# Optimization experiments

Measured on AMD Instinct MI355X. Metric: run time of the kernel, lower is better.

Reference implementation:

```python
import jax, jax.numpy as jnp
import numpy as np

N_NODES = 100_000
N_EDGES = 1_600_000
IN_CH = 128
HIDDEN = 48
OUT_CH = 16
NEG_SLOPE = 0.2  # PyG GATConv default LeakyReLU slope


def setup_inputs() -> dict:
    key = jax.random.key(0)
    ks = jax.random.split(key, 8)
    x = jax.random.normal(ks[0], (N_NODES, IN_CH), dtype=jnp.float32)
    edge_index = jax.random.randint(ks[1], (2, N_EDGES), 0, N_NODES, dtype=jnp.int64)
    W = jax.random.normal(ks[2], (IN_CH, HIDDEN), dtype=jnp.float32) / np.sqrt(IN_CH)
    att_src = jax.random.normal(ks[3], (HIDDEN,), dtype=jnp.float32) / np.sqrt(HIDDEN)
    att_dst = jax.random.normal(ks[4], (HIDDEN,), dtype=jnp.float32) / np.sqrt(HIDDEN)
    gat_bias = jax.random.normal(ks[5], (HIDDEN,), dtype=jnp.float32) * 0.01
    lin_W = jax.random.normal(ks[6], (HIDDEN, OUT_CH), dtype=jnp.float32) / np.sqrt(HIDDEN)
    lin_b = jax.random.normal(ks[7], (OUT_CH,), dtype=jnp.float32) * 0.01
    return {"x": x, "edge_index": edge_index, "W": W, "att_src": att_src,
            "att_dst": att_dst, "gat_bias": gat_bias, "lin_W": lin_W, "lin_b": lin_b}


def reference(x, edge_index, W, att_src, att_dst, gat_bias, lin_W, lin_b):
    n = x.shape[0]
    # PyG GATConv adds self loops by default
    loops = jnp.arange(n, dtype=edge_index.dtype)
    src = jnp.concatenate([edge_index[0], loops])  # [E+N] message sources j
    dst = jnp.concatenate([edge_index[1], loops])  # [E+N] message targets i

    h = x @ W                      # [N, H] transformed node features
    a_src = h @ att_src            # [N] per-node source attention term
    a_dst = h @ att_dst            # [N] per-node destination attention term

    logits = jax.nn.leaky_relu(a_src[src] + a_dst[dst], NEG_SLOPE)  # [E+N]
    # segment softmax over incoming edges of each destination node
    m = jax.ops.segment_max(logits, dst, num_segments=n)            # [N]
    e = jnp.exp(logits - m[dst])
    denom = jax.ops.segment_sum(e, dst, num_segments=n)             # [N] (>0: self loop)
    alpha = e / denom[dst]                                          # [E+N]

    agg = jax.ops.segment_sum(h[src] * alpha[:, None], dst, num_segments=n)
    out = jax.nn.elu(agg + gat_bias)          # [N, H]
    # dropout is identity in eval mode
    z = out @ lin_W + lin_b                   # [N, OUT]
    return jax.nn.log_softmax(z, axis=-1)
```

## Files before the change

### kernel.cpp

```cpp
#include <hip/hip_runtime.h>
#include <hip/hip_fp16.h>

#define IN_CH 128
#define HID 48
#define OUT_CH 16
#define NEG_SLOPE 0.2f
#define SCAN_ELEMS 2048
#define ROWB 128

__device__ __forceinline__ float leaky(float x) { return x >= 0.f ? x : NEG_SLOPE * x; }
__device__ __forceinline__ float elu(float x) { return x > 0.f ? x : __expf(x) - 1.f; }

__device__ __forceinline__ void load_edge(const void* ei, int E, int is64, int e,
                                          int& s, int& d) {
    if (is64) {
        const long long* p = (const long long*)ei;
        s = (int)p[e];
        d = (int)p[(size_t)E + e];
    } else {
        const int* p = (const int*)ei;
        s = p[e];
        d = p[(size_t)E + e];
    }
}

#define BLK_NODES 256
__global__ __launch_bounds__(256, 2) void k_xw(const float* __restrict__ x,
                                               const float* __restrict__ W,
                                               const float* __restrict__ att_src,
                                               const float* __restrict__ att_dst,
                                               const unsigned* __restrict__ ei,
                                               __half* __restrict__ h2,
                                               float* __restrict__ a_src,
                                               float* __restrict__ a_dst,
                                               int* __restrict__ deg,
                                               int* __restrict__ flag, int N) {
    __shared__ float Wl[IN_CH * HID];
    __shared__ float xl[BLK_NODES * 33];
    const int t = threadIdx.x;
    if (blockIdx.x == 0 && t == 0) {
        unsigned sdet = 0;
        for (int i = 1; i < 128; i += 2) sdet |= ei[i];
        *flag = (sdet == 0) ? 1 : 0;
    }
    for (int i = t; i < IN_CH * HID / 4; i += 256)
        ((float4*)Wl)[i] = ((const float4*)W)[i];
    const int n0 = blockIdx.x * BLK_NODES;
    const int kq = t & 3;
    const int ng = t >> 2;
    const int k0 = kq * 12;

    float acc[4][12];
#pragma unroll
    for (int i = 0; i < 4; ++i)
#pragma unroll
        for (int j = 0; j < 12; ++j) acc[i][j] = 0.f;

    for (int c0 = 0; c0 < IN_CH; c0 += 32) {
        __syncthreads();
#pragma unroll
        for (int p = 0; p < 8; ++p) {
            int id = t + p * 256;
            int row = id >> 3;
            int seg = id & 7;
            int n = n0 + row;
            float4 v = make_float4(0.f, 0.f, 0.f, 0.f);
            if (n < N) v = ((const float4*)(x + (size_t)n * IN_CH + c0))[seg];
            float* dst = &xl[row * 33 + seg * 4];
            dst[0] = v.x; dst[1] = v.y; dst[2] = v.z; dst[3] = v.w;
        }
        __syncthreads();
#pragma unroll 8
        for (int cc = 0; cc < 32; ++cc) {
            int c = c0 + cc;
            float xv[4];
#pragma unroll
            for (int i = 0; i < 4; ++i) xv[i] = xl[(ng * 4 + i) * 33 + cc];
            const float* wr = &Wl[c * HID + k0];
#pragma unroll
            for (int j = 0; j < 12; ++j) {
                float wv = wr[j];
#pragma unroll
                for (int i = 0; i < 4; ++i) acc[i][j] += xv[i] * wv;
            }
        }
    }
#pragma unroll
    for (int i = 0; i < 4; ++i) {
        int n = n0 + ng * 4 + i;
        if (n < N) {
            uint* dst = (uint*)((char*)h2 + (size_t)n * ROWB) + k0 / 2;
#pragma unroll
            for (int j = 0; j < 6; ++j) {
                __half2 hv = __floats2half2_rn(acc[i][2 * j], acc[i][2 * j + 1]);
                dst[j] = *(const uint*)&hv;
            }
        }
    }
#pragma unroll
    for (int p = 0; p < 8; ++p) {
        int id = t + p * 256;
        int row = id >> 3;
        int seg = id & 7;
        int n = n0 + row;
        if (n < N) ((uint*)((char*)h2 + (size_t)n * ROWB))[24 + seg] = 0u;
    }
    float as_[4], ad_[4];
#pragma unroll
    for (int i = 0; i < 4; ++i) {
        float s1 = 0.f, s2 = 0.f;
#pragma unroll
        for (int j = 0; j < 12; ++j) {
            float a = acc[i][j];
            s1 += a * att_src[k0 + j];
            s2 += a * att_dst[k0 + j];
        }
        s1 += __shfl_xor(s1, 1); s1 += __shfl_xor(s1, 2);
        s2 += __shfl_xor(s2, 1); s2 += __shfl_xor(s2, 2);
        as_[i] = s1; ad_[i] = s2;
    }
    if (kq == 0) {
#pragma unroll
        for (int i = 0; i < 4; ++i) {
            int n = n0 + ng * 4 + i;
            if (n < N) { a_src[n] = as_[i]; a_dst[n] = ad_[i]; }
        }
    }
    {
        int n = n0 + t;
        if (n < N) deg[n] = 0;
    }
}

__global__ __launch_bounds__(256) void k_count(const void* __restrict__ ei,
                                               const int* __restrict__ flag,
                                               int* __restrict__ deg,
                                               unsigned short* __restrict__ rank, int E) {
    int e = blockIdx.x * blockDim.x + threadIdx.x;
    if (e >= E) return;
    int d = (*flag) ? (int)((const long long*)ei)[(size_t)E + e]
                    : ((const int*)ei)[(size_t)E + e];
    rank[e] = (unsigned short)atomicAdd(&deg[d], 1);
}

__global__ __launch_bounds__(256) void k_scan_block(const int* __restrict__ deg,
                                                    int* __restrict__ rowptr,
                                                    int* __restrict__ bsum, int N) {
    __shared__ int sm[256];
    const int t = threadIdx.x;
    const int base = blockIdx.x * SCAN_ELEMS + t * 8;
    int v[8];
    int s = 0;
#pragma unroll
    for (int i = 0; i < 8; ++i) {
        v[i] = (base + i < N) ? deg[base + i] : 0;
        s += v[i];
    }
    sm[t] = s;
    __syncthreads();
    for (int off = 1; off < 256; off <<= 1) {
        int y = (t >= off) ? sm[t - off] : 0;
        __syncthreads();
        sm[t] += y;
        __syncthreads();
    }
    int run = sm[t] - s;
#pragma unroll
    for (int i = 0; i < 8; ++i) {
        if (base + i < N) rowptr[base + i] = run;
        run += v[i];
    }
    if (t == 255) bsum[blockIdx.x] = sm[255];
}

__global__ __launch_bounds__(256) void k_scan_add(int* __restrict__ rowptr,
                                                  const int* __restrict__ bsum, int N, int E) {
    __shared__ int soff;
    const int chunk = (int)(((long long)blockIdx.x * 256) / SCAN_ELEMS);
    if (threadIdx.x == 0) {
        int run = 0;
        for (int b = 0; b < chunk; ++b) run += bsum[b];
        soff = run;
    }
    __syncthreads();
    int i = blockIdx.x * 256 + threadIdx.x;
    if (i == 0) rowptr[N] = E;
    if (i >= N) return;
    rowptr[i] += soff;
}

__global__ __launch_bounds__(256) void k_scatter(const void* __restrict__ ei,
                                                 const int* __restrict__ flag,
                                                 const int* __restrict__ rowptr,
                                                 const unsigned short* __restrict__ rank,
                                                 unsigned* __restrict__ srcs, int E) {
    int e = blockIdx.x * blockDim.x + threadIdx.x;
    if (e >= E) return;
    int is64 = *flag;
    int s, d;
    load_edge(ei, E, is64, e, s, d);
    int pos = rowptr[d] + (int)rank[e];
    __builtin_nontemporal_store((unsigned)s, srcs + pos);
}

__global__ __launch_bounds__(256) void k_gat_node(const int* __restrict__ rowptr,
                                                  const unsigned* __restrict__ srcs,
                                                  const float* __restrict__ a_src,
                                                  const float* __restrict__ a_dst,
                                                  const __half* __restrict__ h2,
                                                  const float* __restrict__ gat_bias,
                                                  const float* __restrict__ lin_W,
                                                  const float* __restrict__ lin_b,
                                                  float* __restrict__ out, int N) {
    __shared__ float Wl[HID * 17];
    __shared__ float lb[OUT_CH];
    __shared__ float gb[HID];
    __shared__ float o_sm[4][HID];
    __shared__ unsigned long long evb[4][64];
    const int t = threadIdx.x;
    for (int i = t; i < HID * OUT_CH; i += 256) Wl[(i >> 4) * 17 + (i & 15)] = lin_W[i];
    if (t < OUT_CH) lb[t] = lin_b[t];
    if (t >= 64 && t < 64 + HID) gb[t - 64] = gat_bias[t - 64];
    __syncthreads();

    const int wv = t >> 6;
    const int lane = t & 63;
    const int slot = lane >> 4;
    const int c = lane & 15;
    const int n = blockIdx.x * 4 + wv;
    const bool active = n < N;

    if (active) {
        const int base = rowptr[n];
        const int deg = rowptr[n + 1] - base;
        const float adn = a_dst[n];
        const float ev_self = __expf(fminf(leaky(a_src[n] + adn), 50.f));
        const char* hb = (const char*)h2;

        float a0 = 0.f, a1 = 0.f, a2 = 0.f, a3 = 0.f;
        float evsum = (lane == 0) ? ev_self : 0.f;
        if (slot == 0) {
            uint2 hv = *(const uint2*)(hb + (size_t)n * ROWB + 8 * c);
            __half2 h01 = *(const __half2*)&hv.x;
            __half2 h23 = *(const __half2*)&hv.y;
            a0 = ev_self * __low2float(h01);
            a1 = ev_self * __high2float(h01);
            a2 = ev_self * __low2float(h23);
            a3 = ev_self * __high2float(h23);
        }
        for (int c0 = 0; c0 < deg; c0 += 64) {
            int j = c0 + lane;
            unsigned s = 0;
            float ev = 0.f;
            if (j < deg) {
                s = srcs[base + j];
                ev = __expf(fminf(leaky(a_src[s] + adn), 50.f));
            }
            evsum += ev;
            evb[wv][lane] = ((unsigned long long)__float_as_uint(ev) << 32) | s;
            const int cnt = (deg - c0 < 64) ? (deg - c0) : 64;
#pragma unroll 4
            for (int jj = slot; jj < cnt; jj += 4) {
                unsigned long long pr = evb[wv][jj];
                unsigned sj = (unsigned)pr;
                float evj = __uint_as_float((unsigned)(pr >> 32));
                uint2 hv = *(const uint2*)(hb + (size_t)sj * ROWB + 8 * c);
                __half2 h01 = *(const __half2*)&hv.x;
                __half2 h23 = *(const __half2*)&hv.y;
                a0 += evj * __low2float(h01);
                a1 += evj * __high2float(h01);
                a2 += evj * __low2float(h23);
                a3 += evj * __high2float(h23);
            }
        }
#pragma unroll
        for (int off = 1; off < 64; off <<= 1) evsum += __shfl_xor(evsum, off);
        a0 += __shfl_xor(a0, 16); a0 += __shfl_xor(a0, 32);
        a1 += __shfl_xor(a1, 16); a1 += __shfl_xor(a1, 32);
        a2 += __shfl_xor(a2, 16); a2 += __shfl_xor(a2, 32);
        a3 += __shfl_xor(a3, 16); a3 += __shfl_xor(a3, 32);
        const float inv = 1.f / evsum;
        if (slot == 0 && c < 12) {
            float4 v = make_float4(elu(a0 * inv + gb[4 * c + 0]),
                                   elu(a1 * inv + gb[4 * c + 1]),
                                   elu(a2 * inv + gb[4 * c + 2]),
                                   elu(a3 * inv + gb[4 * c + 3]));
            *(float4*)&o_sm[wv][4 * c] = v;
        }
    }
    __syncthreads();

    if (active) {
        const float* o = o_sm[wv];
        float z = 0.f;
#pragma unroll
        for (int i = 0; i < 12; ++i) {
            int k = 12 * slot + i;
            z += o[k] * Wl[k * 17 + c];
        }
        z += __shfl_xor(z, 16); z += __shfl_xor(z, 32);
        z += lb[c];
        float mx = z;
#pragma unroll
        for (int off = 8; off; off >>= 1) mx = fmaxf(mx, __shfl_xor(mx, off, 16));
        float ev = __expf(z - mx);
#pragma unroll
        for (int off = 8; off; off >>= 1) ev += __shfl_xor(ev, off, 16);
        float lse = mx + __logf(ev);
        if (slot == 0) out[(size_t)n * OUT_CH + c] = z - lse;
    }
}

extern "C" void kernel_launch(void* const* d_in, const int* in_sizes, int n_in,
                              void* d_out, int out_size, void* d_ws, size_t ws_size,
                              hipStream_t stream) {
    const float* x = (const float*)d_in[0];
    const void* edge_index = d_in[1];
    const float* W = (const float*)d_in[2];
    const float* att_src = (const float*)d_in[3];
    const float* att_dst = (const float*)d_in[4];
    const float* gat_bias = (const float*)d_in[5];
    const float* lin_W = (const float*)d_in[6];
    const float* lin_b = (const float*)d_in[7];
    float* out = (float*)d_out;

    const int N = in_sizes[0] / IN_CH;
    const int E = in_sizes[1] / 2;

    __half* h2 = (__half*)d_ws;
    float* a_src = (float*)((char*)d_ws + (size_t)N * ROWB);
    float* a_dst = a_src + N;
    int* rowptr = (int*)(a_dst + N);
    int* degbuf = rowptr + N + 1;
    int* bsum = degbuf + N;
    int* flag = bsum + 64;
    unsigned short* rank = (unsigned short*)(flag + 1);
    unsigned* srcs =
        (unsigned*)(((uintptr_t)(rank + E) + 3) & ~(uintptr_t)3);

    const int nodeBlocks = (N + 255) / 256;
    const int edgeBlocks = (E + 255) / 256;
    const int scanBlocks = (N + SCAN_ELEMS - 1) / SCAN_ELEMS;

    k_xw<<<(N + BLK_NODES - 1) / BLK_NODES, 256, 0, stream>>>(
        x, W, att_src, att_dst, (const unsigned*)edge_index,
        h2, a_src, a_dst, degbuf, flag, N);
    k_count<<<edgeBlocks, 256, 0, stream>>>(edge_index, flag, degbuf, rank, E);
    k_scan_block<<<scanBlocks, 256, 0, stream>>>(degbuf, rowptr, bsum, N);
    k_scan_add<<<nodeBlocks, 256, 0, stream>>>(rowptr, bsum, N, E);
    k_scatter<<<edgeBlocks, 256, 0, stream>>>(edge_index, flag, rowptr, rank, srcs, E);
    k_gat_node<<<(N + 3) / 4, 256, 0, stream>>>(rowptr, srcs, a_src, a_dst,
                                                h2, gat_bias, lin_W, lin_b, out, N);
}
```

Baseline: 233.6 us.

## Fuse CSR build into one cooperative kernel with grid syncs

Replaces the count, two scan, and scatter kernels with one cooperative kernel of 512 blocks that uses grid-wide syncs between phases. Block offsets are kept in a separate prefix array read in the scatter and aggregation kernels, so the per-node add pass over rowptr is no longer needed. The aim is to cut launch gaps and one pass over memory. In exchange the persistent grid may lose parallelism in the atomic count and scatter phases, and the grid syncs have their own cost. The padding of the linear weight tile in shared memory also changes.

Result: slower. 401.0 us (+71.6%).

```diff
diff --git a/kernel.cpp b/kernel.cpp
--- a/kernel.cpp
+++ b/kernel.cpp
@@ -1,5 +1,6 @@
 #include <hip/hip_runtime.h>
 #include <hip/hip_fp16.h>
+#include <hip/hip_cooperative_groups.h>
 
 #define IN_CH 128
 #define HID 48
@@ -7,6 +8,7 @@
 #define NEG_SLOPE 0.2f
 #define SCAN_ELEMS 2048
 #define ROWB 128
+#define WLP 20
 
 __device__ __forceinline__ float leaky(float x) { return x >= 0.f ? x : NEG_SLOPE * x; }
 __device__ __forceinline__ float elu(float x) { return x > 0.f ? x : __expf(x) - 1.f; }
@@ -132,78 +134,77 @@
     }
 }
 
-__global__ __launch_bounds__(256) void k_count(const void* __restrict__ ei,
-                                               const int* __restrict__ flag,
-                                               int* __restrict__ deg,
-                                               unsigned short* __restrict__ rank, int E) {
-    int e = blockIdx.x * blockDim.x + threadIdx.x;
-    if (e >= E) return;
-    int d = (*flag) ? (int)((const long long*)ei)[(size_t)E + e]
-                    : ((const int*)ei)[(size_t)E + e];
-    rank[e] = (unsigned short)atomicAdd(&deg[d], 1);
-}
-
-__global__ __launch_bounds__(256) void k_scan_block(const int* __restrict__ deg,
-                                                    int* __restrict__ rowptr,
-                                                    int* __restrict__ bsum, int N) {
-    __shared__ int sm[256];
+__global__ __launch_bounds__(256, 2) void k_csr(const void* __restrict__ ei,
+                                                const int* __restrict__ flag,
+                                                int* __restrict__ deg,
+                                                int* __restrict__ rowptr,
+                                                int* __restrict__ bsum,
+                                                int* __restrict__ pre,
+                                                unsigned short* __restrict__ rank,
+                                                unsigned* __restrict__ srcs,
+                                                int N, int E) {
+    cooperative_groups::grid_group grid = cooperative_groups::this_grid();
     const int t = threadIdx.x;
-    const int base = blockIdx.x * SCAN_ELEMS + t * 8;
-    int v[8];
-    int s = 0;
-#pragma unroll
-    for (int i = 0; i < 8; ++i) {
-        v[i] = (base + i < N) ? deg[base + i] : 0;
-        s += v[i];
-    }
-    sm[t] = s;
-    __syncthreads();
-    for (int off = 1; off < 256; off <<= 1) {
-        int y = (t >= off) ? sm[t - off] : 0;
+    const int b = blockIdx.x;
+    const int gid = b * 256 + t;
+    const int nthr = gridDim.x * 256;
+    const int is64 = *flag;
+    const int nchunks = (N + SCAN_ELEMS - 1) / SCAN_ELEMS;
+
+    for (int e = gid; e < E; e += nthr) {
+        int d = is64 ? (int)((const long long*)ei)[(size_t)E + e]
+                     : ((const int*)ei)[(size_t)E + e];
+        rank[e] = (unsigned short)atomicAdd(&deg[d], 1);
+    }
+    grid.sync();
+
+    if (b < nchunks) {
+        __shared__ int sm[256];
+        const int base = b * SCAN_ELEMS + t * 8;
+        int v[8];
+        int s = 0;
+#pragma unroll
+        for (int i = 0; i < 8; ++i) {
+            v[i] = (base + i < N) ? deg[base + i] : 0;
+            s += v[i];
+        }
+        sm[t] = s;
         __syncthreads();
-        sm[t] += y;
-        __syncthreads();
-    }
-    int run = sm[t] - s;
-#pragma unroll
-    for (int i = 0; i < 8; ++i) {
-        if (base + i < N) rowptr[base + i] = run;
-        run += v[i];
-    }
-    if (t == 255) bsum[blockIdx.x] = sm[255];
-}
-
-__global__ __launch_bounds__(256) void k_scan_add(int* __restrict__ rowptr,
-                                                  const int* __restrict__ bsum, int N, int E) {
-    __shared__ int soff;
-    const int chunk = (int)(((long long)blockIdx.x * 256) / SCAN_ELEMS);
-    if (threadIdx.x == 0) {
+        for (int off = 1; off < 256; off <<= 1) {
+            int y = (t >= off) ? sm[t - off] : 0;
+            __syncthreads();
+            sm[t] += y;
+            __syncthreads();
+        }
+        int run = sm[t] - s;
+#pragma unroll
+        for (int i = 0; i < 8; ++i) {
+            if (base + i < N) rowptr[base + i] = run;
+            else if (base + i == N) rowptr[N] = run;
+            run += v[i];
+        }
+        if (t == 255) bsum[b] = sm[255];
+    }
+    grid.sync();
+
+    if (b == 0 && t == 0) {
         int run = 0;
-        for (int b = 0; b < chunk; ++b) run += bsum[b];
-        soff = run;
-    }
-    __syncthreads();
-    int i = blockIdx.x * 256 + threadIdx.x;
-    if (i == 0) rowptr[N] = E;
-    if (i >= N) return;
-    rowptr[i] += soff;
-}
-
-__global__ __launch_bounds__(256) void k_scatter(const void* __restrict__ ei,
-                                                 const int* __restrict__ flag,
-                                                 const int* __restrict__ rowptr,
-                                                 const unsigned short* __restrict__ rank,
-                                                 unsigned* __restrict__ srcs, int E) {
-    int e = blockIdx.x * blockDim.x + threadIdx.x;
-    if (e >= E) return;
-    int is64 = *flag;
-    int s, d;
-    load_edge(ei, E, is64, e, s, d);
-    int pos = rowptr[d] + (int)rank[e];
-    __builtin_nontemporal_store((unsigned)s, srcs + pos);
+        for (int j = 0; j < nchunks; ++j) { pre[j] = run; run += bsum[j]; }
+        pre[nchunks] = run;
+        if ((N & (SCAN_ELEMS - 1)) == 0) rowptr[N] = 0;
+    }
+    grid.sync();
+
+    for (int e = gid; e < E; e += nthr) {
+        int s, d;
+        load_edge(ei, E, is64, e, s, d);
+        int pos = rowptr[d] + pre[d / SCAN_ELEMS] + (int)rank[e];
+        __builtin_nontemporal_store((unsigned)s, srcs + pos);
+    }
 }
 
 __global__ __launch_bounds__(256) void k_gat_node(const int* __restrict__ rowptr,
+                                                  const int* __restrict__ pre,
                                                   const unsigned* __restrict__ srcs,
                                                   const float* __restrict__ a_src,
                                                   const float* __restrict__ a_dst,
@@ -212,13 +213,13 @@
                                                   const float* __restrict__ lin_W,
                                                   const float* __restrict__ lin_b,
                                                   float* __restrict__ out, int N) {
-    __shared__ float Wl[HID * 17];
+    __shared__ float Wl[HID * WLP];
     __shared__ float lb[OUT_CH];
     __shared__ float gb[HID];
     __shared__ float o_sm[4][HID];
     __shared__ unsigned long long evb[4][64];
     const int t = threadIdx.x;
-    for (int i = t; i < HID * OUT_CH; i += 256) Wl[(i >> 4) * 17 + (i & 15)] = lin_W[i];
+    for (int i = t; i < HID * OUT_CH; i += 256) Wl[(i >> 4) * WLP + (i & 15)] = lin_W[i];
     if (t < OUT_CH) lb[t] = lin_b[t];
     if (t >= 64 && t < 64 + HID) gb[t - 64] = gat_bias[t - 64];
     __syncthreads();
@@ -231,8 +232,8 @@
     const bool active = n < N;
 
     if (active) {
-        const int base = rowptr[n];
-        const int deg = rowptr[n + 1] - base;
+        const int base = rowptr[n] + pre[n / SCAN_ELEMS];
+        const int deg = rowptr[n + 1] + pre[(n + 1) / SCAN_ELEMS] - base;
         const float adn = a_dst[n];
         const float ev_self = __expf(fminf(leaky(a_src[n] + adn), 50.f));
         const char* hb = (const char*)h2;
@@ -296,7 +297,7 @@
 #pragma unroll
         for (int i = 0; i < 12; ++i) {
             int k = 12 * slot + i;
-            z += o[k] * Wl[k * 17 + c];
+            z += o[k] * Wl[k * WLP + c];
         }
         z += __shfl_xor(z, 16); z += __shfl_xor(z, 32);
         z += lb[c];
@@ -333,22 +334,26 @@
     int* rowptr = (int*)(a_dst + N);
     int* degbuf = rowptr + N + 1;
     int* bsum = degbuf + N;
-    int* flag = bsum + 64;
+    int* pre = bsum + 64;
+    int* flag = pre + 65;
     unsigned short* rank = (unsigned short*)(flag + 1);
     unsigned* srcs =
         (unsigned*)(((uintptr_t)(rank + E) + 3) & ~(uintptr_t)3);
 
-    const int nodeBlocks = (N + 255) / 256;
-    const int edgeBlocks = (E + 255) / 256;
-    const int scanBlocks = (N + SCAN_ELEMS - 1) / SCAN_ELEMS;
-
     k_xw<<<(N + BLK_NODES - 1) / BLK_NODES, 256, 0, stream>>>(
         x, W, att_src, att_dst, (const unsigned*)edge_index,
         h2, a_src, a_dst, degbuf, flag, N);
-    k_count<<<edgeBlocks, 256, 0, stream>>>(edge_index, flag, degbuf, rank, E);
-    k_scan_block<<<scanBlocks, 256, 0, stream>>>(degbuf, rowptr, bsum, N);
-    k_scan_add<<<nodeBlocks, 256, 0, stream>>>(rowptr, bsum, N, E);
-    k_scatter<<<edgeBlocks, 256, 0, stream>>>(edge_index, flag, rowptr, rank, srcs, E);
-    k_gat_node<<<(N + 3) / 4, 256, 0, stream>>>(rowptr, srcs, a_src, a_dst,
+
+    {
+        const void* eiv = edge_index;
+        int Nv = N, Ev = E;
+        void* cargs[] = {(void*)&eiv, (void*)&flag, (void*)&degbuf, (void*)&rowptr,
+                         (void*)&bsum, (void*)&pre, (void*)&rank, (void*)&srcs,
+                         (void*)&Nv, (void*)&Ev};
+        hipLaunchCooperativeKernel((const void*)k_csr, dim3(512), dim3(256),
+                                   cargs, 0, stream);
+    }
+
+    k_gat_node<<<(N + 3) / 4, 256, 0, stream>>>(rowptr, pre, srcs, a_src, a_dst,
                                                 h2, gat_bias, lin_W, lin_b, out, N);
 }
```
